# Optimization experiments

Hardware: AMD Instinct MI355X
Metric: run time of the kernel (lower is better)

Reference implementation:

```python
import jax, jax.numpy as jnp
import numpy as np

T, B = 50, 1024
DETER, STOC, EMB, ACT, MLP = 600, 32, 1024, 6, 600
MIN_STD = 0.1

def _p(key, shape):
    return jax.random.normal(key, shape, dtype=jnp.float32) * 0.02

def setup_inputs() -> dict:
    key = jax.random.key(0)
    ks = jax.random.split(key, 20)
    return {
        'actions': jax.random.normal(ks[0], (T, B, ACT), dtype=jnp.float32),
        'nonterminals': jnp.ones((T, B, 1), dtype=jnp.float32),
        'obs_embeddings': jax.random.normal(ks[1], (T, B, EMB), dtype=jnp.float32),
        'noise_prior': jax.random.uniform(ks[2], (T, B, STOC), dtype=jnp.float32),
        'noise_post': jax.random.uniform(ks[3], (T, B, STOC), dtype=jnp.float32),
        'init_deter': jnp.zeros((B, DETER), dtype=jnp.float32),
        'init_stoc': jnp.zeros((B, STOC), dtype=jnp.float32),
        # fc_input: Linear(stoc+action -> deter)
        'W_in': _p(ks[4], (DETER, STOC + ACT)), 'b_in': jnp.zeros((DETER,), jnp.float32),
        # GRUCell(deter, deter): torch layout [3*H, in]
        'W_ih': _p(ks[5], (3 * DETER, DETER)), 'b_ih': jnp.zeros((3 * DETER,), jnp.float32),
        'W_hh': _p(ks[6], (3 * DETER, DETER)), 'b_hh': jnp.zeros((3 * DETER,), jnp.float32),
        # fc_prior: deter -> mlp -> 2*stoc
        'Wp1': _p(ks[7], (MLP, DETER)), 'bp1': jnp.zeros((MLP,), jnp.float32),
        'Wp2': _p(ks[8], (2 * STOC, MLP)), 'bp2': jnp.zeros((2 * STOC,), jnp.float32),
        # fc_posterior: deter+emb -> mlp -> 2*stoc
        'Wq1': _p(ks[9], (MLP, DETER + EMB)), 'bq1': jnp.zeros((MLP,), jnp.float32),
        'Wq2': _p(ks[10], (2 * STOC, MLP)), 'bq2': jnp.zeros((2 * STOC,), jnp.float32),
    }

def _rollout(actions, nonterminals, obs_embeddings, noise_prior, noise_post,
             init_deter, init_stoc, W_in, b_in, W_ih, b_ih, W_hh, b_hh,
             Wp1, bp1, Wp2, bp2, Wq1, bq1, Wq2, bq2):
    def step(carry, inp):
        deter, stoc = carry
        a, nt, emb, n_p, n_q = inp
        # fc_input + ELU
        x = jax.nn.elu(jnp.concatenate([stoc * nt, a], axis=-1) @ W_in.T + b_in)
        # torch GRUCell
        gi = x @ W_ih.T + b_ih            # [B, 3D]
        gh = deter @ W_hh.T + b_hh        # [B, 3D]
        ir, iz, inn = jnp.split(gi, 3, axis=-1)
        hr, hz, hn = jnp.split(gh, 3, axis=-1)
        r = jax.nn.sigmoid(ir + hr)
        z = jax.nn.sigmoid(iz + hz)
        n = jnp.tanh(inn + r * hn)
        h = (1.0 - z) * n + z * deter
        # prior head
        pp = jax.nn.elu(h @ Wp1.T + bp1) @ Wp2.T + bp2
        p_mu, p_std = jnp.split(pp, 2, axis=-1)
        p_std = jax.nn.softplus(p_std) + MIN_STD
        p_stoc = p_mu + p_std * n_p  # uniform noise, matching torch.rand_like
        # posterior head
        qq = jax.nn.elu(jnp.concatenate([h, emb], axis=-1) @ Wq1.T + bq1) @ Wq2.T + bq2
        q_mu, q_std = jnp.split(qq, 2, axis=-1)
        q_std = jax.nn.softplus(q_std) + MIN_STD
        q_stoc = q_mu + q_std * n_q
        out = jnp.concatenate([h, p_mu, p_std, p_stoc, q_mu, q_std, q_stoc], axis=-1)
        return (h, q_stoc), out

    _, outs = jax.lax.scan(step, (init_deter, init_stoc),
                           (actions, nonterminals, obs_embeddings, noise_prior, noise_post))
    return outs  # [T, B, DETER + 6*STOC]

def reference(actions, nonterminals, obs_embeddings, noise_prior, noise_post,
              init_deter, init_stoc, W_in, b_in, W_ih, b_ih, W_hh, b_hh,
              Wp1, bp1, Wp2, bp2, Wq1, bq1, Wq2, bq2):
    return _rollout(actions, nonterminals, obs_embeddings, noise_prior, noise_post,
                    init_deter, init_stoc, W_in, b_in, W_ih, b_ih, W_hh, b_hh,
                    Wp1, bp1, Wp2, bp2, Wq1, bq1, Wq2, bq2)
```

## Files before the change

kernel.cpp:

```cpp
#include <hip/hip_runtime.h>

typedef __bf16 bf16x8 __attribute__((ext_vector_type(8)));
typedef float f32x4 __attribute__((ext_vector_type(4)));
typedef unsigned short u16;
typedef unsigned int u32;
typedef unsigned long long u64;

#define NT 50
#define NB 1024
#define DET 600
#define DP 608
#define NP 640
#define HLD 640
#define EMB 1024
#define OUTW 792
#define GBLK 160
#define HXS2 ((size_t)NB * HLD)

__device__ __forceinline__ u16 f2bf(float f) {
  unsigned u = __float_as_uint(f);
  u += 0x7FFFu + ((u >> 16) & 1u);
  return (u16)(u >> 16);
}
__device__ __forceinline__ float bf2f(u16 h) { return __uint_as_float(((unsigned)h) << 16); }
__device__ __forceinline__ float eluf(float x) { return x > 0.f ? x : expm1f(x); }
__device__ __forceinline__ float sigm(float x) { return 1.f / (1.f + expf(-x)); }
__device__ __forceinline__ float softplusf(float x) {
  return fmaxf(x, 0.f) + log1pf(expf(-fabsf(x)));
}

__device__ __forceinline__ void gll16(const void* g, void* l) {
  __builtin_amdgcn_global_load_lds(
      (const __attribute__((address_space(1))) u32*)g,
      (__attribute__((address_space(3))) u32*)l, 16, 0, 0);
}

__device__ __forceinline__ u32 ld32sc(const u32* p_) {
  return __hip_atomic_load(p_, __ATOMIC_RELAXED, __HIP_MEMORY_SCOPE_SYSTEM);
}
__device__ __forceinline__ void st32sc(u32* p_, u32 v) {
  __hip_atomic_store(p_, v, __ATOMIC_RELAXED, __HIP_MEMORY_SCOPE_SYSTEM);
}

__device__ __forceinline__ u32 ldflag(const u32* bar, int i, u32 target) {
  return (i >= 1 && i < GBLK) ? ld32sc(&bar[i]) : target;
}
__device__ __forceinline__ void gridbar(u32* bar, u32 target) {
  __syncthreads();
  if (blockIdx.x == 0) {
    if (threadIdx.x < 64) {
      const int l = threadIdx.x;
      for (;;) {
        u32 a = ldflag(bar, l, target);
        u32 b = ldflag(bar, l + 64, target);
        u32 c = ldflag(bar, l + 128, target);
        u32 mn = min(min(a, b), c);
        if (__all(mn >= target)) break;
        __builtin_amdgcn_s_sleep(2);
      }
      if (l == 0) st32sc(&bar[GBLK + 32], target);
    }
  } else if (threadIdx.x == 0) {
    st32sc(&bar[blockIdx.x], target);
    while (ld32sc(&bar[GBLK + 32]) < target)
      __builtin_amdgcn_s_sleep(2);
  }
  __syncthreads();
}


struct PK {
  const u16 *W6, *Wp1, *Wq1h, *Wp2, *Wq2, *Winp, *QE;
  const float *b_ih, *b_hh, *bp1, *bq1, *bp2, *bq2, *b_in;
  const float *init_deter, *actions, *nonterm, *noise_p, *noise_q;
  u16 *xbuf, *hbuf;
  float *out;
  u32 *bar;
};

__global__ __launch_bounds__(256, 1) void rssm_persist(PK p)
{
  __shared__ char smem[65536] __attribute__((aligned(16)));

  const int bid = blockIdx.x, tid = threadIdx.x;
  const int lane = tid & 63, w = tid >> 6;
  const int r16 = lane & 15, k8g = lane >> 4;

  const int xg = bid & 7, gg = bid >> 3;
  const int my = (gg & 3) * 4 + (xg >> 1);
  const int nx = (gg >> 2) * 2 + (xg & 1);
  const int Am0 = my * 64, An0 = nx * 64;
  const int wr = w >> 1, wc = w & 1;
  const int srow = tid >> 2;
  const int sk8 = ((tid & 3) - ((tid >> 3) & 3)) & 3;
  const int lo = w * 1024;
  const u16* bw[6];
#pragma unroll
  for (int s = 0; s < 6; s++)
    bw[s] = p.W6 + (size_t)s * NP * DP + (size_t)(An0 + srow) * DP + sk8 * 8;
  const size_t aoff = (size_t)(Am0 + srow) * HLD + sk8 * 8;

  const bool doB = bid < 128;
  const int slice = bid >> 1, head = bid & 1;
  const int Bm0 = slice * 16;
  const u16* W1 = head ? p.Wq1h : p.Wp1;
  const float* b1 = head ? p.bq1 : p.bp1;
  const u16* W2 = head ? p.Wq2 : p.Wp2;
  const float* b2 = head ? p.bq2 : p.bp2;

  u16* hsl = (u16*)smem;
  u16* ph  = (u16*)(smem + 19712);
  float* red = (float*)(smem + 40448);
  u16* xin = (u16*)(smem + 52736);

  for (int t = 0; t < NT; ++t) {
    const u16* hprev = p.hbuf + (size_t)t * HXS2;
    u16* hnow = p.hbuf + (size_t)(t + 1) * HXS2;
    const u16* xcur = p.xbuf + (size_t)t * HXS2;
    u16* xnxt = p.xbuf + (size_t)(t + 1) * HXS2;
    float* out_t = p.out + (size_t)t * NB * OUTW;

    {
      const u16* axp = xcur + aoff;
      const u16* ahp = hprev + aoff;
      auto ldsT = [&](int buf, int tile) -> char* { return smem + buf * 32768 + tile * 4096; };
      f32x4 acc[6][2][2] = {};
      auto stage = [&](int buf, int kc) {
        gll16(axp + kc, ldsT(buf, 0) + lo);
        gll16(ahp + kc, ldsT(buf, 1) + lo);
#pragma unroll
        for (int s = 0; s < 6; s++) gll16(bw[s] + kc, ldsT(buf, 2 + s) + lo);
      };
      auto compute = [&](int buf) {
        bf16x8 ax_[2], ah_[2];
#pragma unroll
        for (int i = 0; i < 2; i++) {
          int row = wr * 32 + i * 16 + r16;
          int S = row * 4 + ((k8g + (row >> 1)) & 3);
          ax_[i] = *(const bf16x8*)(ldsT(buf, 0) + S * 16);
          ah_[i] = *(const bf16x8*)(ldsT(buf, 1) + S * 16);
        }
#pragma unroll
        for (int s = 0; s < 6; s++) {
#pragma unroll
          for (int j = 0; j < 2; j++) {
            int row = wc * 32 + j * 16 + r16;
            int S = row * 4 + ((k8g + (row >> 1)) & 3);
            bf16x8 b = *(const bf16x8*)(ldsT(buf, 2 + s) + S * 16);
#pragma unroll
            for (int i = 0; i < 2; i++)
              acc[s][i][j] = __builtin_amdgcn_mfma_f32_16x16x32_bf16(
                  (s < 3) ? ax_[i] : ah_[i], b, acc[s][i][j], 0, 0, 0);
          }
        }
      };
      stage(0, 0);
      for (int it = 0; it < 19; ++it) {
        if (it + 1 < 19) {
          stage((it + 1) & 1, (it + 1) * 32);
          asm volatile("s_waitcnt vmcnt(8)" ::: "memory");
        } else {
          asm volatile("s_waitcnt vmcnt(0)" ::: "memory");
        }
        __builtin_amdgcn_s_barrier();
        __builtin_amdgcn_sched_barrier(0);
        compute(it & 1);
        __builtin_amdgcn_s_barrier();
      }
      const float* dprev = t ? (out_t - (size_t)NB * OUTW) : p.init_deter;
      const int dstr = t ? OUTW : DET;
#pragma unroll
      for (int j = 0; j < 2; j++) {
        int n = An0 + wc * 32 + j * 16 + r16;
        bool nok = (n < DET);
        float bihr = nok ? p.b_ih[n] : 0.f, bhhr = nok ? p.b_hh[n] : 0.f;
        float bihz = nok ? p.b_ih[600 + n] : 0.f, bhhz = nok ? p.b_hh[600 + n] : 0.f;
        float bihn = nok ? p.b_ih[1200 + n] : 0.f, bhhn = nok ? p.b_hh[1200 + n] : 0.f;
#pragma unroll
        for (int i = 0; i < 2; i++) {
          int mb = Am0 + wr * 32 + i * 16 + k8g * 4;
#pragma unroll
          for (int r = 0; r < 4; r++) {
            int m = mb + r;
            float dp = nok ? dprev[(size_t)m * dstr + n] : 0.f;
            float rg = sigm(acc[0][i][j][r] + bihr + acc[3][i][j][r] + bhhr);
            float zg = sigm(acc[1][i][j][r] + bihz + acc[4][i][j][r] + bhhz);
            float ng = tanhf(acc[2][i][j][r] + bihn + rg * (acc[5][i][j][r] + bhhn));
            float h = (1.f - zg) * ng + zg * dp;
            u32 hb16 = f2bf(h);
            u32 other = (u32)__shfl_xor((int)hb16, 1, 64);
            if (nok) {
              out_t[(size_t)m * OUTW + n] = h;
              if (!(lane & 1))
                st32sc((u32*)&hnow[(size_t)m * HLD + n], hb16 | (other << 16));
            }
          }
        }
      }
    }
    gridbar(p.bar, 2 * t + 1);

    if (doB) {
      const bool donext = (t + 1 < NT);
      const float* noise = (head ? p.noise_q : p.noise_p) + (size_t)t * NB * 32;

      {
        const u16* hrow = hnow + (size_t)Bm0 * HLD;
#pragma unroll
        for (int c = 0; c < 5; ++c) {
          int chunk = c * 256 + tid;
          char* ldst = (char*)hsl + (c * 256 + w * 64) * 16;
          if (chunk < 1232) {
            int row = chunk / 77, cc = chunk - row * 77;
            int scc = cc < 76 ? cc : 75;
            gll16(hrow + (size_t)row * HLD + scc * 8, ldst);
          }
        }
      }
      float qe[10][4] = {};
      if (head) {
        const u16* qbase = p.QE + ((size_t)t * NB + Bm0) * NP;
#pragma unroll
        for (int i = 0; i < 10; i++) {
          int j = w + i * 4;
          if (j < 38) {
            int n = j * 16 + r16;
#pragma unroll
            for (int r = 0; r < 4; r++)
              qe[i][r] = bf2f(qbase[(size_t)(k8g * 4 + r) * NP + n]);
          }
        }
      }
      for (int i = tid; i < 320; i += 256) {
        int r = i / 20, c = i - r * 20;
        *(u32*)&ph[r * 648 + 608 + 2 * c] = 0;
      }
      if (donext)
        for (int i = tid; i < 576; i += 256) ((u32*)xin)[i] = 0;
      __syncthreads();

      f32x4 a1[10] = {};
      for (int kc = 0; kc < DP; kc += 32) {
        bf16x8 fa = *(const bf16x8*)&hsl[r16 * 616 + kc + k8g * 8];
#pragma unroll
        for (int i = 0; i < 10; i++) {
          int j = w + i * 4;
          if (j < 38) {
            bf16x8 fb = *(const bf16x8*)&W1[(size_t)(j * 16 + r16) * DP + kc + k8g * 8];
            a1[i] = __builtin_amdgcn_mfma_f32_16x16x32_bf16(fa, fb, a1[i], 0, 0, 0);
          }
        }
      }
#pragma unroll
      for (int i = 0; i < 10; i++) {
        int j = w + i * 4;
        if (j >= 38) break;
        int n = j * 16 + r16;
#pragma unroll
        for (int r = 0; r < 4; r++) {
          int mrow = k8g * 4 + r;
          float v = a1[i][r];
          if (n < DET) {
            v += b1[n] + qe[i][r];
            ph[mrow * 648 + n] = f2bf(eluf(v));
          } else {
            ph[mrow * 648 + n] = 0;
          }
        }
      }
      __syncthreads();
      f32x4 a2[4] = {};
      {
        int kc0 = w * 160;
#pragma unroll
        for (int ks = 0; ks < 5; ks++) {
          int kc = kc0 + ks * 32;
          bf16x8 fa = *(const bf16x8*)&ph[r16 * 648 + kc + k8g * 8];
#pragma unroll
          for (int j = 0; j < 4; j++) {
            bf16x8 fb = *(const bf16x8*)&W2[(size_t)(j * 16 + r16) * NP + kc + k8g * 8];
            a2[j] = __builtin_amdgcn_mfma_f32_16x16x32_bf16(fa, fb, a2[j], 0, 0, 0);
          }
        }
      }
      if (w) {
#pragma unroll
        for (int j = 0; j < 4; j++)
#pragma unroll
          for (int r = 0; r < 4; r++)
            red[(w - 1) * 1024 + (j * 16 + r16) * 16 + k8g * 4 + r] = a2[j][r];
      }
      __syncthreads();
      if (w == 0) {
#pragma unroll
        for (int j = 0; j < 4; j++)
#pragma unroll
          for (int r = 0; r < 4; r++) {
            int c = j * 16 + r16, mr = k8g * 4 + r;
            a2[j][r] += red[c * 16 + mr] + red[1024 + c * 16 + mr] + red[2048 + c * 16 + mr];
          }
        const int ob = head ? 696 : 600;
        const float* ntn = donext ? p.nonterm + (size_t)(t + 1) * NB : nullptr;
#pragma unroll
        for (int j = 0; j < 2; j++) {
          int c = j * 16 + r16;
          float bmu = b2[c], bsd = b2[32 + c];
#pragma unroll
          for (int r = 0; r < 4; r++) {
            int mr = k8g * 4 + r, m = Bm0 + mr;
            float mu = a2[j][r] + bmu;
            float sd = softplusf(a2[j + 2][r] + bsd) + 0.1f;
            float st = mu + sd * noise[(size_t)m * 32 + c];
            float* op = out_t + (size_t)m * OUTW + ob;
            op[c] = mu; op[32 + c] = sd; op[64 + c] = st;
            if (head && donext) xin[mr * 72 + c] = f2bf(st * ntn[m]);
          }
        }
      } else if (w == 1 && head && donext) {
        const float* an = p.actions + (size_t)(t + 1) * NB * 6;
#pragma unroll
        for (int rep = 0; rep < 2; rep++) {
          int idx = lane + rep * 64;
          if (idx < 96) {
            int rr = idx / 6, c = idx - rr * 6;
            xin[rr * 72 + 32 + c] = f2bf(an[(size_t)(Bm0 + rr) * 6 + c]);
          }
        }
      }
      if (head && donext) {
        __syncthreads();
        f32x4 xc[10] = {};
        const int nb = w * 160;
#pragma unroll
        for (int kc = 0; kc < 64; kc += 32) {
          bf16x8 fa = *(const bf16x8*)&xin[r16 * 72 + kc + k8g * 8];
#pragma unroll
          for (int j = 0; j < 10; j++) {
            bf16x8 fb = *(const bf16x8*)&p.Winp[(size_t)(nb + j * 16 + r16) * 64 + kc + k8g * 8];
            xc[j] = __builtin_amdgcn_mfma_f32_16x16x32_bf16(fa, fb, xc[j], 0, 0, 0);
          }
        }
#pragma unroll
        for (int j = 0; j < 10; j++) {
          int n = nb + j * 16 + r16;
          bool nok = (n < DET);
          float bi = nok ? p.b_in[n] : 0.f;
#pragma unroll
          for (int r = 0; r < 4; r++) {
            int m = Bm0 + k8g * 4 + r;
            float v = eluf(xc[j][r] + bi);
            u32 xb16 = f2bf(v);
            u32 other = (u32)__shfl_xor((int)xb16, 1, 64);
            if (nok && !(lane & 1))
              st32sc((u32*)&xnxt[(size_t)m * HLD + n], xb16 | (other << 16));
          }
        }
      }
    }
    if (t + 1 < NT) gridbar(p.bar, 2 * t + 2);
  }
}

struct GemmZ {
  const u16* A; int lda;
  const u16* B; int ldb;
  int K;
  const float* bias;
  u16* C; int ldc;
  int mode;
};

__global__ __launch_bounds__(256, 2) void gemmP(GemmZ g)
{
  __shared__ u16 lA[2][128 * 32];
  __shared__ u16 lB[2][128 * 32];
  const int tid = threadIdx.x, lane = tid & 63, w = tid >> 6;
  const int wr = w >> 1, wc = w & 1;
  const size_t m0 = (size_t)blockIdx.y * 128;
  const int n0 = blockIdx.x * 128;
  const int r16 = lane & 15, k8g = lane >> 4;
  f32x4 acc[4][4] = {};

  const int S0 = tid, S1 = tid + 256;
  const int ar0 = S0 >> 2, ak0 = (((S0 & 3) - ((S0 >> 3) & 3)) & 3) * 8;
  const int ar1 = S1 >> 2, ak1 = (((S1 & 3) - ((S1 >> 3) & 3)) & 3) * 8;
  const int lo = w * 1024;
  const int niter = g.K / 32;

  auto stage = [&](int buf, int kc) {
    gll16(g.A + (m0 + ar0) * (size_t)g.lda + kc + ak0, (char*)lA[buf] + lo);
    gll16(g.A + (m0 + ar1) * (size_t)g.lda + kc + ak1, (char*)lA[buf] + 4096 + lo);
    gll16(g.B + (size_t)(n0 + ar0) * g.ldb + kc + ak0, (char*)lB[buf] + lo);
    gll16(g.B + (size_t)(n0 + ar1) * g.ldb + kc + ak1, (char*)lB[buf] + 4096 + lo);
  };
  auto compute = [&](int buf) {
    bf16x8 fa[4], fb[4];
#pragma unroll
    for (int i = 0; i < 4; i++) {
      int row = wr * 64 + i * 16 + r16;
      int S = row * 4 + ((k8g + (row >> 1)) & 3);
      fa[i] = *(const bf16x8*)((const char*)lA[buf] + S * 16);
    }
#pragma unroll
    for (int j = 0; j < 4; j++) {
      int row = wc * 64 + j * 16 + r16;
      int S = row * 4 + ((k8g + (row >> 1)) & 3);
      fb[j] = *(const bf16x8*)((const char*)lB[buf] + S * 16);
    }
#pragma unroll
    for (int i = 0; i < 4; i++)
#pragma unroll
      for (int j = 0; j < 4; j++)
        acc[i][j] = __builtin_amdgcn_mfma_f32_16x16x32_bf16(fa[i], fb[j], acc[i][j], 0, 0, 0);
  };

  stage(0, 0);
  __syncthreads();
  for (int it = 0; it < niter; ++it) {
    if (it + 1 < niter) stage((it + 1) & 1, (it + 1) * 32);
    compute(it & 1);
    __syncthreads();
  }

#pragma unroll
  for (int i = 0; i < 4; i++) {
    size_t mb = m0 + wr * 64 + i * 16 + k8g * 4;
#pragma unroll
    for (int j = 0; j < 4; j++) {
      int n = n0 + wc * 64 + j * 16 + r16;
      if (g.mode == 1) {
        if (n >= DP) continue;
        float b = (n < DET) ? g.bias[n] : 0.f;
#pragma unroll
        for (int r = 0; r < 4; r++)
          g.C[(mb + r) * (size_t)g.ldc + n] = f2bf(eluf(acc[i][j][r] + b));
      } else {
        if (n >= g.ldc) continue;
#pragma unroll
        for (int r = 0; r < 4; r++)
          g.C[(mb + r) * (size_t)g.ldc + n] = f2bf(acc[i][j][r]);
      }
    }
  }
}

__global__ void wconv_k(const float* src, int srows, int scols, int sstride,
                        u16* dst, int drows, int dstride, int c0, int cw)
{
  int idx = blockIdx.x * 256 + threadIdx.x;
  if (idx >= drows * cw) return;
  int r = idx / cw, c = idx - r * cw;
  float v = (r < srows && c < scols) ? src[(size_t)r * sstride + c] : 0.f;
  dst[(size_t)r * dstride + c0 + c] = f2bf(v);
}

__global__ void conv8_k(const float* src, u16* dst, int n8)
{
  int i = blockIdx.x * 256 + threadIdx.x;
  if (i >= n8) return;
  const float4* s = (const float4*)(src + (size_t)i * 8);
  float4 f0 = s[0], f1 = s[1];
  union { u16 h[8]; int4 v; } cv;
  cv.h[0] = f2bf(f0.x); cv.h[1] = f2bf(f0.y); cv.h[2] = f2bf(f0.z); cv.h[3] = f2bf(f0.w);
  cv.h[4] = f2bf(f1.x); cv.h[5] = f2bf(f1.y); cv.h[6] = f2bf(f1.z); cv.h[7] = f2bf(f1.w);
  *(int4*)(dst + (size_t)i * 8) = cv.v;
}

__global__ void xin0_k(const float* stoc0, const float* nt0, const float* act0, u16* xing)
{
  int i = blockIdx.x * 256 + threadIdx.x;
  if (i >= NB * 64) return;
  int m = i >> 6, c = i & 63;
  float v = 0.f;
  if (c < 32) v = stoc0[m * 32 + c] * nt0[m];
  else if (c < 38) v = act0[m * 6 + (c - 32)];
  xing[i] = f2bf(v);
}

extern "C" void kernel_launch(void* const* d_in, const int* in_sizes, int n_in,
                              void* d_out, int out_size, void* d_ws, size_t ws_size,
                              hipStream_t stream)
{
  const float* actions    = (const float*)d_in[0];
  const float* nonterm    = (const float*)d_in[1];
  const float* emb        = (const float*)d_in[2];
  const float* noise_p    = (const float*)d_in[3];
  const float* noise_q    = (const float*)d_in[4];
  const float* init_deter = (const float*)d_in[5];
  const float* init_stoc  = (const float*)d_in[6];
  const float* W_in = (const float*)d_in[7];
  const float* b_in = (const float*)d_in[8];
  const float* W_ih = (const float*)d_in[9];
  const float* b_ih = (const float*)d_in[10];
  const float* W_hh = (const float*)d_in[11];
  const float* b_hh = (const float*)d_in[12];
  const float* Wp1 = (const float*)d_in[13];
  const float* bp1 = (const float*)d_in[14];
  const float* Wp2 = (const float*)d_in[15];
  const float* bp2 = (const float*)d_in[16];
  const float* Wq1 = (const float*)d_in[17];
  const float* bq1 = (const float*)d_in[18];
  const float* Wq2 = (const float*)d_in[19];
  const float* bq2 = (const float*)d_in[20];
  float* out = (float*)d_out;

  char* wsp = (char*)d_ws;
  size_t o = 0;
  auto alloc = [&](size_t b) { char* pp = wsp + o; o = (o + b + 255) & ~(size_t)255; return pp; };
  u16* W6   = (u16*)alloc(6ull * NP * DP * 2);
  u16* Wp1p = (u16*)alloc((size_t)NP * DP * 2);
  u16* Wq1h = (u16*)alloc((size_t)NP * DP * 2);
  u16* Wq1e = (u16*)alloc((size_t)NP * EMB * 2);
  u16* Wp2p = (u16*)alloc(64ull * NP * 2);
  u16* Wq2p = (u16*)alloc(64ull * NP * 2);
  u16* Winp = (u16*)alloc((size_t)NP * 64 * 2);
  u16* xing = (u16*)alloc((size_t)NB * 64 * 2);
  u32* barp = (u32*)alloc(4096);
  u16* xbuf = (u16*)alloc(HXS2 * 2 * (NT + 1));
  u16* hbuf = (u16*)alloc(HXS2 * 2 * (NT + 1));
  u16* embb = (u16*)alloc((size_t)NT * NB * EMB * 2);
  u16* QE   = (u16*)alloc((size_t)NT * NB * NP * 2);
  if (o > ws_size) return;

  hipMemsetAsync(barp, 0, 4096, stream);

  auto wcl = [&](const float* src, int sr, int sc, int ss, u16* dst, int dr, int ds, int c0, int cw) {
    int n = dr * cw;
    wconv_k<<<(n + 255) / 256, 256, 0, stream>>>(src, sr, sc, ss, dst, dr, ds, c0, cw);
  };
  for (int s = 0; s < 3; s++) {
    wcl(W_ih + (size_t)s * 600 * 600, 600, 600, 600, W6 + (size_t)s * NP * DP, NP, DP, 0, DP);
    wcl(W_hh + (size_t)s * 600 * 600, 600, 600, 600, W6 + (size_t)(3 + s) * NP * DP, NP, DP, 0, DP);
  }
  wcl(Wp1, 600, 600, 600, Wp1p, NP, DP, 0, DP);
  wcl(Wq1, 600, 600, 1624, Wq1h, NP, DP, 0, DP);
  wcl(Wq1 + 600, 600, 1024, 1624, Wq1e, NP, EMB, 0, EMB);
  wcl(Wp2, 64, 600, 600, Wp2p, 64, NP, 0, NP);
  wcl(Wq2, 64, 600, 600, Wq2p, 64, NP, 0, NP);
  wcl(W_in, 600, 38, 38, Winp, NP, 64, 0, 64);
  wcl(init_deter, 1024, 600, 600, hbuf, 1024, HLD, 0, DP);

  {
    int n8 = NT * NB * EMB / 8;
    conv8_k<<<(n8 + 255) / 256, 256, 0, stream>>>(emb, embb, n8);
    GemmZ gq = { embb, EMB, Wq1e, EMB, EMB, nullptr, QE, NP, 2 };
    gemmP<<<dim3(5, 400, 1), 256, 0, stream>>>(gq);
  }
  xin0_k<<<NB * 64 / 256, 256, 0, stream>>>(init_stoc, nonterm, actions, xing);
  {
    GemmZ gx = { xing, 64, Winp, 64, 64, b_in, xbuf, HLD, 1 };
    gemmP<<<dim3(5, 8, 1), 256, 0, stream>>>(gx);
  }

  PK pk = { W6, Wp1p, Wq1h, Wp2p, Wq2p, Winp, QE,
            b_ih, b_hh, bp1, bq1, bp2, bq2, b_in,
            init_deter, actions, nonterm, noise_p, noise_q,
            xbuf, hbuf, out, barp };
  rssm_persist<<<GBLK, 256, 0, stream>>>(pk);
}
```

Baseline: 5.583 ms.

## Repartition persistent RSSM kernel into 768 smaller blocks at three per CU

The persistent kernel grows from 160 to 768 blocks. The GRU GEMM tile shrinks from 64x64 to 32 rows by 26 columns, and each head block now handles 8 batch rows instead of 16. Shared memory is halved so three blocks fit per CU, with buffers aliased and the head reduction folded into the epilogue. The aim is to fill all CUs and hide latency better. The cost is a grid barrier that now polls 768 flags, less reuse per tile, and some MFMA lanes wasted on the 26-of-32 column and 8-of-16 row padding.

```diff
diff --git a/kernel.cpp b/kernel.cpp
--- a/kernel.cpp
+++ b/kernel.cpp
@@ -14,7 +14,9 @@
 #define HLD 640
 #define EMB 1024
 #define OUTW 792
-#define GBLK 160
+#define GBLK 768
+#define NG 24
+#define NCOLS 26
 #define HXS2 ((size_t)NB * HLD)
 
 __device__ __forceinline__ u16 f2bf(float f) {
@@ -42,28 +44,27 @@
   __hip_atomic_store(p_, v, __ATOMIC_RELAXED, __HIP_MEMORY_SCOPE_SYSTEM);
 }
 
-__device__ __forceinline__ u32 ldflag(const u32* bar, int i, u32 target) {
-  return (i >= 1 && i < GBLK) ? ld32sc(&bar[i]) : target;
-}
 __device__ __forceinline__ void gridbar(u32* bar, u32 target) {
   __syncthreads();
   if (blockIdx.x == 0) {
     if (threadIdx.x < 64) {
       const int l = threadIdx.x;
       for (;;) {
-        u32 a = ldflag(bar, l, target);
-        u32 b = ldflag(bar, l + 64, target);
-        u32 c = ldflag(bar, l + 128, target);
-        u32 mn = min(min(a, b), c);
+        u32 mn = 0xFFFFFFFFu;
+#pragma unroll
+        for (int k = 0; k < 12; k++) {
+          int idx = l + k * 64;
+          u32 v = (idx >= 1 && idx < GBLK) ? ld32sc(&bar[idx]) : target;
+          mn = min(mn, v);
+        }
         if (__all(mn >= target)) break;
         __builtin_amdgcn_s_sleep(2);
       }
-      if (l == 0) st32sc(&bar[GBLK + 32], target);
+      if (l == 0) st32sc(&bar[960], target);
     }
   } else if (threadIdx.x == 0) {
     st32sc(&bar[blockIdx.x], target);
-    while (ld32sc(&bar[GBLK + 32]) < target)
-      __builtin_amdgcn_s_sleep(2);
+    while (ld32sc(&bar[960]) < target) __builtin_amdgcn_s_sleep(2);
   }
   __syncthreads();
 }
@@ -78,40 +79,47 @@
   u32 *bar;
 };
 
-__global__ __launch_bounds__(256, 1) void rssm_persist(PK p)
+__global__ __launch_bounds__(256, 3) void rssm_persist(PK p)
 {
-  __shared__ char smem[65536] __attribute__((aligned(16)));
+  __shared__ char smem[32768] __attribute__((aligned(16)));
 
   const int bid = blockIdx.x, tid = threadIdx.x;
   const int lane = tid & 63, w = tid >> 6;
   const int r16 = lane & 15, k8g = lane >> 4;
 
-  const int xg = bid & 7, gg = bid >> 3;
-  const int my = (gg & 3) * 4 + (xg >> 1);
-  const int nx = (gg >> 2) * 2 + (xg & 1);
-  const int Am0 = my * 64, An0 = nx * 64;
+  const int my = bid / NG, ng = bid - my * NG;
+  const int Am0 = my * 32, nbase = ng * NCOLS;
   const int wr = w >> 1, wc = w & 1;
-  const int srow = tid >> 2;
-  const int sk8 = ((tid & 3) - ((tid >> 3) & 3)) & 3;
-  const int lo = w * 1024;
-  const u16* bw[6];
-#pragma unroll
-  for (int s = 0; s < 6; s++)
-    bw[s] = p.W6 + (size_t)s * NP * DP + (size_t)(An0 + srow) * DP + sk8 * 8;
-  const size_t aoff = (size_t)(Am0 + srow) * HLD + sk8 * 8;
-
-  const bool doB = bid < 128;
+
+  int skind[4]; size_t ssrc[4]; u32 sdst[4];
+#pragma unroll
+  for (int q = 0; q < 4; q++) {
+    int u = w * 4 + q;
+    int S = (u & 1) * 64 + lane;
+    int row = S >> 2;
+    int k8 = ((S & 3) - ((S >> 3) & 3)) & 3;
+    int tile = u >> 1;
+    sdst[q] = tile * 2048 + (u & 1) * 1024;
+    if (tile < 2) {
+      skind[q] = tile;
+      ssrc[q] = (size_t)(Am0 + row) * HLD + k8 * 8;
+    } else {
+      skind[q] = 2;
+      ssrc[q] = (size_t)(tile - 2) * NP * DP + (size_t)(nbase + row) * DP + k8 * 8;
+    }
+  }
+
+  const bool doB = bid < 256;
   const int slice = bid >> 1, head = bid & 1;
-  const int Bm0 = slice * 16;
+  const int Bm0 = slice * 8;
   const u16* W1 = head ? p.Wq1h : p.Wp1;
   const float* b1 = head ? p.bq1 : p.bp1;
   const u16* W2 = head ? p.Wq2 : p.Wp2;
   const float* b2 = head ? p.bq2 : p.bp2;
 
-  u16* hsl = (u16*)smem;
-  u16* ph  = (u16*)(smem + 19712);
-  float* red = (float*)(smem + 40448);
-  u16* xin = (u16*)(smem + 52736);
+  u16* hslph = (u16*)smem;
+  float* red = (float*)(smem + 20736);
+  u16* xin = (u16*)(smem + 26880);
 
   for (int t = 0; t < NT; ++t) {
     const u16* hprev = p.hbuf + (size_t)t * HXS2;
@@ -121,44 +129,34 @@
     float* out_t = p.out + (size_t)t * NB * OUTW;
 
     {
-      const u16* axp = xcur + aoff;
-      const u16* ahp = hprev + aoff;
-      auto ldsT = [&](int buf, int tile) -> char* { return smem + buf * 32768 + tile * 4096; };
-      f32x4 acc[6][2][2] = {};
+      f32x4 acc[6] = {};
       auto stage = [&](int buf, int kc) {
-        gll16(axp + kc, ldsT(buf, 0) + lo);
-        gll16(ahp + kc, ldsT(buf, 1) + lo);
-#pragma unroll
-        for (int s = 0; s < 6; s++) gll16(bw[s] + kc, ldsT(buf, 2 + s) + lo);
+#pragma unroll
+        for (int q = 0; q < 4; q++) {
+          const u16* mat = (skind[q] == 0) ? xcur : (skind[q] == 1) ? hprev : p.W6;
+          gll16(mat + ssrc[q] + kc, smem + buf * 16384 + sdst[q]);
+        }
       };
       auto compute = [&](int buf) {
-        bf16x8 ax_[2], ah_[2];
-#pragma unroll
-        for (int i = 0; i < 2; i++) {
-          int row = wr * 32 + i * 16 + r16;
-          int S = row * 4 + ((k8g + (row >> 1)) & 3);
-          ax_[i] = *(const bf16x8*)(ldsT(buf, 0) + S * 16);
-          ah_[i] = *(const bf16x8*)(ldsT(buf, 1) + S * 16);
-        }
+        const char* base = smem + buf * 16384;
+        int rowa = wr * 16 + r16;
+        int Sa = rowa * 4 + ((k8g + (rowa >> 1)) & 3);
+        bf16x8 ax = *(const bf16x8*)(base + Sa * 16);
+        bf16x8 ah = *(const bf16x8*)(base + 2048 + Sa * 16);
+        int rowb = wc * 16 + r16;
+        int Sb = rowb * 4 + ((k8g + (rowb >> 1)) & 3);
 #pragma unroll
         for (int s = 0; s < 6; s++) {
-#pragma unroll
-          for (int j = 0; j < 2; j++) {
-            int row = wc * 32 + j * 16 + r16;
-            int S = row * 4 + ((k8g + (row >> 1)) & 3);
-            bf16x8 b = *(const bf16x8*)(ldsT(buf, 2 + s) + S * 16);
-#pragma unroll
-            for (int i = 0; i < 2; i++)
-              acc[s][i][j] = __builtin_amdgcn_mfma_f32_16x16x32_bf16(
-                  (s < 3) ? ax_[i] : ah_[i], b, acc[s][i][j], 0, 0, 0);
-          }
+          bf16x8 b = *(const bf16x8*)(base + 4096 + s * 2048 + Sb * 16);
+          acc[s] = __builtin_amdgcn_mfma_f32_16x16x32_bf16(
+              (s < 3) ? ax : ah, b, acc[s], 0, 0, 0);
         }
       };
       stage(0, 0);
       for (int it = 0; it < 19; ++it) {
         if (it + 1 < 19) {
           stage((it + 1) & 1, (it + 1) * 32);
-          asm volatile("s_waitcnt vmcnt(8)" ::: "memory");
+          asm volatile("s_waitcnt vmcnt(4)" ::: "memory");
         } else {
           asm volatile("s_waitcnt vmcnt(0)" ::: "memory");
         }
@@ -169,32 +167,26 @@
       }
       const float* dprev = t ? (out_t - (size_t)NB * OUTW) : p.init_deter;
       const int dstr = t ? OUTW : DET;
-#pragma unroll
-      for (int j = 0; j < 2; j++) {
-        int n = An0 + wc * 32 + j * 16 + r16;
-        bool nok = (n < DET);
-        float bihr = nok ? p.b_ih[n] : 0.f, bhhr = nok ? p.b_hh[n] : 0.f;
-        float bihz = nok ? p.b_ih[600 + n] : 0.f, bhhz = nok ? p.b_hh[600 + n] : 0.f;
-        float bihn = nok ? p.b_ih[1200 + n] : 0.f, bhhn = nok ? p.b_hh[1200 + n] : 0.f;
-#pragma unroll
-        for (int i = 0; i < 2; i++) {
-          int mb = Am0 + wr * 32 + i * 16 + k8g * 4;
-#pragma unroll
-          for (int r = 0; r < 4; r++) {
-            int m = mb + r;
-            float dp = nok ? dprev[(size_t)m * dstr + n] : 0.f;
-            float rg = sigm(acc[0][i][j][r] + bihr + acc[3][i][j][r] + bhhr);
-            float zg = sigm(acc[1][i][j][r] + bihz + acc[4][i][j][r] + bhhz);
-            float ng = tanhf(acc[2][i][j][r] + bihn + rg * (acc[5][i][j][r] + bhhn));
-            float h = (1.f - zg) * ng + zg * dp;
-            u32 hb16 = f2bf(h);
-            u32 other = (u32)__shfl_xor((int)hb16, 1, 64);
-            if (nok) {
-              out_t[(size_t)m * OUTW + n] = h;
-              if (!(lane & 1))
-                st32sc((u32*)&hnow[(size_t)m * HLD + n], hb16 | (other << 16));
-            }
-          }
+      const int local = wc * 16 + r16;
+      const int n = nbase + local;
+      const bool nok = (local < NCOLS) && (n < DET);
+      float bihr = nok ? p.b_ih[n] : 0.f, bhhr = nok ? p.b_hh[n] : 0.f;
+      float bihz = nok ? p.b_ih[600 + n] : 0.f, bhhz = nok ? p.b_hh[600 + n] : 0.f;
+      float bihn = nok ? p.b_ih[1200 + n] : 0.f, bhhn = nok ? p.b_hh[1200 + n] : 0.f;
+#pragma unroll
+      for (int r = 0; r < 4; r++) {
+        int m = Am0 + wr * 16 + k8g * 4 + r;
+        float dp = nok ? dprev[(size_t)m * dstr + n] : 0.f;
+        float rg = sigm(acc[0][r] + bihr + acc[3][r] + bhhr);
+        float zg = sigm(acc[1][r] + bihz + acc[4][r] + bhhz);
+        float ngt = tanhf(acc[2][r] + bihn + rg * (acc[5][r] + bhhn));
+        float h = (1.f - zg) * ngt + zg * dp;
+        u32 hb16 = f2bf(h);
+        u32 other = (u32)__shfl_xor((int)hb16, 1, 64);
+        if (nok) {
+          out_t[(size_t)m * OUTW + n] = h;
+          if (!(lane & 1))
+            st32sc((u32*)&hnow[(size_t)m * HLD + n], hb16 | (other << 16));
         }
       }
     }
@@ -207,14 +199,12 @@
       {
         const u16* hrow = hnow + (size_t)Bm0 * HLD;
 #pragma unroll
-        for (int c = 0; c < 5; ++c) {
+        for (int c = 0; c < 3; ++c) {
           int chunk = c * 256 + tid;
-          char* ldst = (char*)hsl + (c * 256 + w * 64) * 16;
-          if (chunk < 1232) {
-            int row = chunk / 77, cc = chunk - row * 77;
-            int scc = cc < 76 ? cc : 75;
-            gll16(hrow + (size_t)row * HLD + scc * 8, ldst);
-          }
+          int ch2 = chunk < 616 ? chunk : 615;
+          int row = ch2 / 77, cc = ch2 - row * 77;
+          gll16(hrow + (size_t)row * HLD + cc * 8,
+                smem + (c * 256 + w * 64) * 16);
         }
       }
       float qe[10][4] = {};
@@ -226,14 +216,12 @@
           if (j < 38) {
             int n = j * 16 + r16;
 #pragma unroll
-            for (int r = 0; r < 4; r++)
-              qe[i][r] = bf2f(qbase[(size_t)(k8g * 4 + r) * NP + n]);
-          }
-        }
-      }
-      for (int i = tid; i < 320; i += 256) {
-        int r = i / 20, c = i - r * 20;
-        *(u32*)&ph[r * 648 + 608 + 2 * c] = 0;
+            for (int r = 0; r < 4; r++) {
+              int mr = k8g * 4 + r;
+              if (mr < 8) qe[i][r] = bf2f(qbase[(size_t)mr * NP + n]);
+            }
+          }
+        }
       }
       if (donext)
         for (int i = tid; i < 576; i += 256) ((u32*)xin)[i] = 0;
@@ -241,7 +229,7 @@
 
       f32x4 a1[10] = {};
       for (int kc = 0; kc < DP; kc += 32) {
-        bf16x8 fa = *(const bf16x8*)&hsl[r16 * 616 + kc + k8g * 8];
+        bf16x8 fa = *(const bf16x8*)&hslph[r16 * 616 + kc + k8g * 8];
 #pragma unroll
         for (int i = 0; i < 10; i++) {
           int j = w + i * 4;
@@ -251,21 +239,18 @@
           }
         }
       }
+      __syncthreads();
 #pragma unroll
       for (int i = 0; i < 10; i++) {
         int j = w + i * 4;
         if (j >= 38) break;
         int n = j * 16 + r16;
+        if (n >= DET) continue;
 #pragma unroll
         for (int r = 0; r < 4; r++) {
           int mrow = k8g * 4 + r;
-          float v = a1[i][r];
-          if (n < DET) {
-            v += b1[n] + qe[i][r];
-            ph[mrow * 648 + n] = f2bf(eluf(v));
-          } else {
-            ph[mrow * 648 + n] = 0;
-          }
+          float v = a1[i][r] + b1[n] + qe[i][r];
+          hslph[mrow * 648 + n] = f2bf(eluf(v));
         }
       }
       __syncthreads();
@@ -275,7 +260,7 @@
 #pragma unroll
         for (int ks = 0; ks < 5; ks++) {
           int kc = kc0 + ks * 32;
-          bf16x8 fa = *(const bf16x8*)&ph[r16 * 648 + kc + k8g * 8];
+          bf16x8 fa = *(const bf16x8*)&hslph[r16 * 648 + kc + k8g * 8];
 #pragma unroll
           for (int j = 0; j < 4; j++) {
             bf16x8 fb = *(const bf16x8*)&W2[(size_t)(j * 16 + r16) * NP + kc + k8g * 8];
@@ -287,18 +272,13 @@
 #pragma unroll
         for (int j = 0; j < 4; j++)
 #pragma unroll
-          for (int r = 0; r < 4; r++)
-            red[(w - 1) * 1024 + (j * 16 + r16) * 16 + k8g * 4 + r] = a2[j][r];
+          for (int r = 0; r < 4; r++) {
+            int mr = k8g * 4 + r;
+            if (mr < 8) red[(w - 1) * 512 + (j * 16 + r16) * 8 + mr] = a2[j][r];
+          }
       }
       __syncthreads();
       if (w == 0) {
-#pragma unroll
-        for (int j = 0; j < 4; j++)
-#pragma unroll
-          for (int r = 0; r < 4; r++) {
-            int c = j * 16 + r16, mr = k8g * 4 + r;
-            a2[j][r] += red[c * 16 + mr] + red[1024 + c * 16 + mr] + red[2048 + c * 16 + mr];
-          }
         const int ob = head ? 696 : 600;
         const float* ntn = donext ? p.nonterm + (size_t)(t + 1) * NB : nullptr;
 #pragma unroll
@@ -307,9 +287,14 @@
           float bmu = b2[c], bsd = b2[32 + c];
 #pragma unroll
           for (int r = 0; r < 4; r++) {
-            int mr = k8g * 4 + r, m = Bm0 + mr;
-            float mu = a2[j][r] + bmu;
-            float sd = softplusf(a2[j + 2][r] + bsd) + 0.1f;
+            int mr = k8g * 4 + r;
+            if (mr >= 8) continue;
+            int m = Bm0 + mr;
+            float mu = a2[j][r] + red[c * 8 + mr] + red[512 + c * 8 + mr]
+                     + red[1024 + c * 8 + mr] + bmu;
+            float s2 = a2[j + 2][r] + red[(32 + c) * 8 + mr]
+                     + red[512 + (32 + c) * 8 + mr] + red[1024 + (32 + c) * 8 + mr] + bsd;
+            float sd = softplusf(s2) + 0.1f;
             float st = mu + sd * noise[(size_t)m * 32 + c];
             float* op = out_t + (size_t)m * OUTW + ob;
             op[c] = mu; op[32 + c] = sd; op[64 + c] = st;
@@ -318,13 +303,9 @@
         }
       } else if (w == 1 && head && donext) {
         const float* an = p.actions + (size_t)(t + 1) * NB * 6;
-#pragma unroll
-        for (int rep = 0; rep < 2; rep++) {
-          int idx = lane + rep * 64;
-          if (idx < 96) {
-            int rr = idx / 6, c = idx - rr * 6;
-            xin[rr * 72 + 32 + c] = f2bf(an[(size_t)(Bm0 + rr) * 6 + c]);
-          }
+        if (lane < 48) {
+          int rr = lane / 6, cc = lane - rr * 6;
+          xin[rr * 72 + 32 + cc] = f2bf(an[(size_t)(Bm0 + rr) * 6 + cc]);
         }
       }
       if (head && donext) {
@@ -347,12 +328,12 @@
           float bi = nok ? p.b_in[n] : 0.f;
 #pragma unroll
           for (int r = 0; r < 4; r++) {
-            int m = Bm0 + k8g * 4 + r;
+            int mr = k8g * 4 + r;
             float v = eluf(xc[j][r] + bi);
             u32 xb16 = f2bf(v);
             u32 other = (u32)__shfl_xor((int)xb16, 1, 64);
-            if (nok && !(lane & 1))
-              st32sc((u32*)&xnxt[(size_t)m * HLD + n], xb16 | (other << 16));
+            if (nok && mr < 8 && !(lane & 1))
+              st32sc((u32*)&xnxt[(size_t)(Bm0 + mr) * HLD + n], xb16 | (other << 16));
           }
         }
       }
```

Result: slower. 7.153 ms (+28.1%).
